# Performance work log

Measured on AMD Instinct MI355X. Metric: run time of the kernel, lower is better.

## Reference

```python
import jax, jax.numpy as jnp
import numpy as np

D_STATE = 64
D_CONV = 4
DT_RANK = 16  # ceil(256/16)
LN_EPS = 1e-5


def _mamba_layer(x, ln_g, ln_b, in_w, conv_w, conv_b, xp_w, dt_w, dt_b, A_log, Dp, out_w):
    B, L, d_model = x.shape
    # LayerNorm (pre-norm)
    mu = x.mean(-1, keepdims=True)
    var = ((x - mu) ** 2).mean(-1, keepdims=True)
    xn = (x - mu) * jax.lax.rsqrt(var + LN_EPS) * ln_g + ln_b
    # in_proj -> split into x-branch and gate z
    xz = xn @ in_w.T                    # [B,L,2*d_inner]
    xm, z = jnp.split(xz, 2, axis=-1)   # each [B,L,d_inner]
    d_inner = xm.shape[-1]
    # causal depthwise conv1d (kernel D_CONV), then SiLU
    xp = jnp.pad(xm, ((0, 0), (D_CONV - 1, 0), (0, 0)))
    xc = conv_b + sum(xp[:, k:k + L, :] * conv_w[:, k] for k in range(D_CONV))
    xc = jax.nn.silu(xc)
    # input-dependent SSM params
    dbl = xc @ xp_w.T                   # [B,L,dt_rank+2*N]
    dt, Bm, Cm = jnp.split(dbl, [DT_RANK, DT_RANK + D_STATE], axis=-1)
    dt = jax.nn.softplus(dt @ dt_w.T + dt_b)   # [B,L,d_inner]
    A = -jnp.exp(A_log)                 # [d_inner, N]

    def step(h, inp):
        dt_t, B_t, C_t, u_t = inp       # [B,Di],[B,N],[B,N],[B,Di]
        dA = jnp.exp(dt_t[:, :, None] * A)                 # [B,Di,N]
        dBu = (dt_t * u_t)[:, :, None] * B_t[:, None, :]   # [B,Di,N]
        h = dA * h + dBu
        y = jnp.einsum('bdn,bn->bd', h, C_t)
        return h, y

    h0 = jnp.zeros((B, d_inner, D_STATE), x.dtype)
    _, ys = jax.lax.scan(
        step, h0,
        (dt.transpose(1, 0, 2), Bm.transpose(1, 0, 2), Cm.transpose(1, 0, 2), xc.transpose(1, 0, 2)))
    y = ys.transpose(1, 0, 2) + xc * Dp  # skip term D*u
    y = y * jax.nn.silu(z)               # gating
    out = y @ out_w.T                    # out_proj
    return out + x                       # residual


def reference(x, ln_g, ln_b, in_w, conv_w, conv_b, xp_w, dt_w, dt_b, A_log, Dp, out_w):
    depth = ln_g.shape[0]
    for i in range(depth):
        x = _mamba_layer(x, ln_g[i], ln_b[i], in_w[i], conv_w[i], conv_b[i],
                         xp_w[i], dt_w[i], dt_b[i], A_log[i], Dp[i], out_w[i])
    return x


def setup_inputs() -> dict:
    key = jax.random.key(0)
    ks = jax.random.split(key, 8)
    B, L, d_model, depth = 4, 1024, 256, 2
    d_inner = 2 * d_model
    x = jax.random.normal(ks[0], (B, L, d_model), jnp.float32)
    s = 0.02
    in_w = jax.random.normal(ks[1], (depth, 2 * d_inner, d_model), jnp.float32) * s
    conv_w = jax.random.normal(ks[2], (depth, d_inner, D_CONV), jnp.float32) * 0.3
    conv_b = jnp.zeros((depth, d_inner), jnp.float32)
    xp_w = jax.random.normal(ks[3], (depth, DT_RANK + 2 * D_STATE, d_inner), jnp.float32) * s
    dt_w = jax.random.normal(ks[4], (depth, d_inner, DT_RANK), jnp.float32) * 0.1
    # inverse-softplus of ~0.01 so dt starts small (mamba-style init)
    dt_b = jnp.full((depth, d_inner), float(np.log(np.expm1(0.01))), jnp.float32)
    # A = diag(1..N) per channel -> A_log = log(arange)
    A_log = jnp.broadcast_to(jnp.log(jnp.arange(1, D_STATE + 1, dtype=jnp.float32)),
                             (depth, d_inner, D_STATE))
    Dp = jnp.ones((depth, d_inner), jnp.float32)
    out_w = jax.random.normal(ks[5], (depth, d_model, d_inner), jnp.float32) * s
    ln_g = jnp.ones((depth, d_model), jnp.float32)
    ln_b = jnp.zeros((depth, d_model), jnp.float32)
    return {"x": x, "ln_g": ln_g, "ln_b": ln_b, "in_w": in_w, "conv_w": conv_w,
            "conv_b": conv_b, "xp_w": xp_w, "dt_w": dt_w, "dt_b": dt_b,
            "A_log": A_log, "Dp": Dp, "out_w": out_w}
```

## Files before the change

### kernel.cpp

```cpp
#include <hip/hip_runtime.h>
#include <math.h>

#define DI 512
#define DM 256
#define LSEQ 1024
#define BB 4
#define NST 64
#define ROWS (BB*LSEQ)
#define NC 16
#define CL 64

typedef __bf16 bf16x8 __attribute__((ext_vector_type(8)));
typedef __bf16 bf16x4 __attribute__((ext_vector_type(4)));
typedef float f32x4 __attribute__((ext_vector_type(4)));
typedef unsigned short u16;
typedef u16 u16x8 __attribute__((ext_vector_type(8)));
typedef int i32x2 __attribute__((ext_vector_type(2)));

__device__ __forceinline__ float siluf(float x) { return x / (1.f + __expf(-x)); }
__device__ __forceinline__ float softplusf(float x) { return (x > 20.f) ? x : log1pf(__expf(x)); }
__device__ __forceinline__ float rlane(float v, int l) {
    return __int_as_float(__builtin_amdgcn_readlane(__float_as_int(v), l));
}
__device__ __forceinline__ float fexp2(float x) {
#if __has_builtin(__builtin_amdgcn_exp2f)
    return __builtin_amdgcn_exp2f(x);
#else
    return __expf(x * 0.69314718056f);
#endif
}
template<int PAT>
__device__ __forceinline__ float fswz(float v) {
    return __int_as_float(__builtin_amdgcn_ds_swizzle(__float_as_int(v), PAT));
}

__device__ __forceinline__ float tree8(const float (&s)[8], int lane) {
    const bool b4 = (lane & 16) != 0;
    const bool b3 = (lane & 8) != 0;
    float r[4];
#if __has_builtin(__builtin_amdgcn_permlane32_swap)
    #pragma unroll
    for (int i = 0; i < 4; ++i) {
        i32x2 pr = __builtin_amdgcn_permlane32_swap(
            __float_as_int(s[i]), __float_as_int(s[i+4]), false, false);
        r[i] = __int_as_float(pr[0]) + __int_as_float(pr[1]);
    }
#else
    const bool b5 = (lane & 32) != 0;
    #pragma unroll
    for (int i = 0; i < 4; ++i) {
        float u = b5 ? s[i+4] : s[i];
        float w = b5 ? s[i]   : s[i+4];
        r[i] = u + __shfl_xor(w, 32, 64);
    }
#endif
    float q[2];
    #pragma unroll
    for (int i = 0; i < 2; ++i) {
        float u = b4 ? r[i+2] : r[i];
        float w = b4 ? r[i]   : r[i+2];
        q[i] = u + fswz<0x401F>(w);
    }
    float u = b3 ? q[1] : q[0];
    float w = b3 ? q[0] : q[1];
    float p = u + fswz<0x201F>(w);
    p += fswz<0x101F>(p);
    p += fswz<0x081F>(p);
    p += fswz<0x041F>(p);
    return p;
}

__global__ __launch_bounds__(256) void f2bf(
    const float* __restrict__ in, __bf16* __restrict__ out, int n)
{
    int i = (blockIdx.x * 256 + threadIdx.x) * 4;
    if (i >= n) return;
    float4 v = *(const float4*)(in + i);
    bf16x4 o;
    o[0] = (__bf16)v.x; o[1] = (__bf16)v.y; o[2] = (__bf16)v.z; o[3] = (__bf16)v.w;
    *(bf16x4*)(out + i) = o;
}

__global__ __launch_bounds__(256) void ln_kernel(
    const float* __restrict__ x, const float* __restrict__ g,
    const float* __restrict__ b, __bf16* __restrict__ xn)
{
    int lane = threadIdx.x & 63;
    int row = blockIdx.x * 4 + (threadIdx.x >> 6);
    const float4* xr = (const float4*)(x + (size_t)row * DM);
    float4 v = xr[lane];
    float s = v.x + v.y + v.z + v.w;
    #pragma unroll
    for (int o = 32; o; o >>= 1) s += __shfl_xor(s, o, 64);
    float mu = s * (1.f / DM);
    float dx = v.x - mu, dy = v.y - mu, dz = v.z - mu, dw = v.w - mu;
    float q = dx*dx + dy*dy + dz*dz + dw*dw;
    #pragma unroll
    for (int o = 32; o; o >>= 1) q += __shfl_xor(q, o, 64);
    float inv = rsqrtf(q * (1.f / DM) + 1e-5f);
    float4 gv = ((const float4*)g)[lane];
    float4 bv = ((const float4*)b)[lane];
    bf16x4 o4;
    o4[0] = (__bf16)(dx * inv * gv.x + bv.x);
    o4[1] = (__bf16)(dy * inv * gv.y + bv.y);
    o4[2] = (__bf16)(dz * inv * gv.z + bv.z);
    o4[3] = (__bf16)(dw * inv * gv.w + bv.w);
    *(bf16x4*)(xn + (size_t)row * DM + lane * 4) = o4;
}

template<int KK>
__global__ __launch_bounds__(256) void gemm_mfma(
    const __bf16* __restrict__ A, const __bf16* __restrict__ W,
    float* __restrict__ C, __bf16* __restrict__ C2b,
    const float* __restrict__ res, int N, int mode)
{
    int wid = threadIdx.x >> 6, lane = threadIdx.x & 63;
    int wr = wid >> 1, wc = wid & 1;
    int bm = blockIdx.y * 64, bn = blockIdx.x * 64;
    int l15 = lane & 15, lk = (lane >> 4) * 8;
    const __bf16* Ap = A + (size_t)(bm + wr*32 + l15) * KK + lk;
    int wrow0 = bn + wc*32 + l15;
    int wrow1 = wrow0 + 16;
    if (wrow0 > N-1) wrow0 = N-1;
    if (wrow1 > N-1) wrow1 = N-1;
    const __bf16* Wp0 = W + (size_t)wrow0 * KK + lk;
    const __bf16* Wp1 = W + (size_t)wrow1 * KK + lk;
    f32x4 acc[2][2] = {};
    #pragma unroll 4
    for (int k0 = 0; k0 < KK; k0 += 32) {
        bf16x8 b0 = *(const bf16x8*)(Wp0 + k0);
        bf16x8 b1 = *(const bf16x8*)(Wp1 + k0);
        #pragma unroll
        for (int m = 0; m < 2; ++m) {
            bf16x8 a = *(const bf16x8*)(Ap + (size_t)m*16*KK + k0);
            acc[m][0] = __builtin_amdgcn_mfma_f32_16x16x32_bf16(a, b0, acc[m][0], 0, 0, 0);
            acc[m][1] = __builtin_amdgcn_mfma_f32_16x16x32_bf16(a, b1, acc[m][1], 0, 0, 0);
        }
    }
    int r4 = (lane >> 4) * 4;
    #pragma unroll
    for (int m = 0; m < 2; ++m) {
        int row = bm + wr*32 + m*16 + r4;
        #pragma unroll
        for (int n = 0; n < 2; ++n) {
            int col = bn + wc*32 + n*16 + l15;
            #pragma unroll
            for (int r = 0; r < 4; ++r) {
                float v = acc[m][n][r];
                int rr = row + r;
                if (mode == 0) {
                    if (col < N) C[(size_t)rr * N + col] = v;
                } else if (mode == 1) {
                    if (col < 512) C[(size_t)rr * 512 + col] = v;
                    else           C2b[(size_t)rr * 512 + col - 512] = (__bf16)v;
                } else {
                    C[(size_t)rr * N + col] = v + res[(size_t)rr * N + col];
                }
            }
        }
    }
}

__global__ __launch_bounds__(256) void gemm_dt(
    const float* __restrict__ A, int lda,
    const float* __restrict__ W,
    float* __restrict__ CT, const float* __restrict__ aux)
{
    __shared__ float As[16][68];
    __shared__ float Ws[16][68];
    const int bm = blockIdx.y * 64;
    const int bn = blockIdx.x * 64;
    const int tid = threadIdx.x;
    const int tx = tid & 15;
    const int ty = tid >> 4;
    const int lr = tid >> 2;
    const int lc = (tid & 3) << 2;
    float acc[4][4] = {};
    {
        float4 av = *(const float4*)(A + (size_t)(bm + lr) * lda + lc);
        float4 wv = *(const float4*)(W + (size_t)(bn + lr) * 16 + lc);
        As[lc+0][lr] = av.x; As[lc+1][lr] = av.y; As[lc+2][lr] = av.z; As[lc+3][lr] = av.w;
        Ws[lc+0][lr] = wv.x; Ws[lc+1][lr] = wv.y; Ws[lc+2][lr] = wv.z; Ws[lc+3][lr] = wv.w;
        __syncthreads();
        #pragma unroll
        for (int k = 0; k < 16; ++k) {
            float a[4], w[4];
            #pragma unroll
            for (int i = 0; i < 4; ++i) a[i] = As[k][ty*4 + i];
            #pragma unroll
            for (int j = 0; j < 4; ++j) w[j] = Ws[k][tx*4 + j];
            #pragma unroll
            for (int i = 0; i < 4; ++i)
                #pragma unroll
                for (int j = 0; j < 4; ++j)
                    acc[i][j] = fmaf(a[i], w[j], acc[i][j]);
        }
    }
    #pragma unroll
    for (int j = 0; j < 4; ++j) {
        int n = bn + tx*4 + j;
        float bia = aux[n];
        float4 v;
        v.x = softplusf(acc[0][j] + bia);
        v.y = softplusf(acc[1][j] + bia);
        v.z = softplusf(acc[2][j] + bia);
        v.w = softplusf(acc[3][j] + bia);
        *(float4*)(CT + (size_t)n * ROWS + bm + ty*4) = v;
    }
}

__global__ __launch_bounds__(256) void conv_tr_kernel(
    const float* __restrict__ xm, const float* __restrict__ cw,
    const float* __restrict__ cb, const u16* __restrict__ zin,
    __bf16* __restrict__ xcb, u16* __restrict__ xcT, u16* __restrict__ zT)
{
    __shared__ float xs[67][66];
    __shared__ u16 Tc[64][72];
    __shared__ u16 Tz[64][72];
    const int tid = threadIdx.x;
    const int row0 = blockIdx.y * 64;
    const int d0 = blockIdx.x * 64;
    #pragma unroll
    for (int it = 0; it < 5; ++it) {
        int f4 = it * 256 + tid;
        if (f4 < 67 * 16) {
            int rr = f4 >> 4;
            int cc = (f4 & 15) * 4;
            int g = row0 - 3 + rr;
            float4 v = make_float4(0.f, 0.f, 0.f, 0.f);
            if (g >= 0 && (g >> 10) == (row0 >> 10))
                v = *(const float4*)(xm + (size_t)g * DI + d0 + cc);
            *(float4*)&xs[rr][cc] = v;
        }
    }
    const int r = tid >> 2;
    const int c0 = (tid & 3) * 16;
    {
        const u16* zp = zin + (size_t)(row0 + r) * DI + d0 + c0;
        *(u16x8*)&Tz[r][c0]     = *(const u16x8*)(zp);
        *(u16x8*)&Tz[r][c0 + 8] = *(const u16x8*)(zp + 8);
    }
    __syncthreads();
    {
        bf16x8 v0, v1;
        #pragma unroll
        for (int j = 0; j < 16; ++j) {
            int d = d0 + c0 + j;
            float acc = cb[d]
                + xs[r+0][c0+j] * cw[d*4+0]
                + xs[r+1][c0+j] * cw[d*4+1]
                + xs[r+2][c0+j] * cw[d*4+2]
                + xs[r+3][c0+j] * cw[d*4+3];
            __bf16 o = (__bf16)siluf(acc);
            if (j < 8) v0[j] = o; else v1[j-8] = o;
            Tc[r][c0+j] = *(const u16*)&o;
        }
        __bf16* op = xcb + (size_t)(row0 + r) * DI + d0 + c0;
        *(bf16x8*)(op)     = v0;
        *(bf16x8*)(op + 8) = v1;
    }
    __syncthreads();
    {
        u16x8 a0, a1, b0, b1;
        #pragma unroll
        for (int i = 0; i < 8; ++i) {
            a0[i] = Tc[c0+i][r];   a1[i] = Tc[c0+8+i][r];
            b0[i] = Tz[c0+i][r];   b1[i] = Tz[c0+8+i][r];
        }
        u16* oc = xcT + (size_t)(d0 + r) * ROWS + row0 + c0;
        u16* oz = zT  + (size_t)(d0 + r) * ROWS + row0 + c0;
        *(u16x8*)(oc)     = a0;
        *(u16x8*)(oc + 8) = a1;
        *(u16x8*)(oz)     = b0;
        *(u16x8*)(oz + 8) = b1;
    }
}

__global__ __launch_bounds__(256) void transpose_bf(
    const u16* __restrict__ in, u16* __restrict__ out, int ldi, int ldo)
{
    __shared__ u16 tile[64][72];
    int r = threadIdx.x >> 2;
    int c0 = (threadIdx.x & 3) * 16;
    const u16* ip = in + (size_t)(blockIdx.y*64 + r) * ldi + blockIdx.x*64 + c0;
    *(u16x8*)&tile[r][c0]     = *(const u16x8*)(ip);
    *(u16x8*)&tile[r][c0 + 8] = *(const u16x8*)(ip + 8);
    __syncthreads();
    u16* op = out + (size_t)(blockIdx.x*64 + r) * ldo + blockIdx.y*64 + c0;
    u16x8 v0, v1;
    #pragma unroll
    for (int i = 0; i < 8; ++i) { v0[i] = tile[c0+i][r]; v1[i] = tile[c0+8+i][r]; }
    *(u16x8*)(op)     = v0;
    *(u16x8*)(op + 8) = v1;
}

__global__ __launch_bounds__(256) void scan_p1T(
    const float* __restrict__ dtT, const __bf16* __restrict__ xcT,
    const float* __restrict__ dbl, const float* __restrict__ A_log,
    float* __restrict__ Pe, float* __restrict__ He)
{
    int wid = (blockIdx.x * 256 + threadIdx.x) >> 6;
    int lane = threadIdx.x & 63;
    int c = wid & (NC - 1);
    int d = (wid >> 4) & (DI - 1);
    int b = wid >> 13;
    float An2 = -__expf(A_log[d * NST + lane]) * 1.44269504f;
    size_t row0 = (size_t)b * LSEQ + (size_t)c * CL;
    size_t tix = (size_t)d * ROWS + row0;
    float dtv = dtT[tix + lane];
    float uvf = (float)xcT[tix + lane];
    float duv = dtv * uvf;
    float Sdt = dtv;
    #pragma unroll
    for (int o = 32; o; o >>= 1) Sdt += __shfl_xor(Sdt, o, 64);
    const float* bp = dbl + row0 * 144 + 16 + lane;
    float H = 0.f;
    #pragma unroll
    for (int j = 0; j < 8; ++j) {
        #pragma unroll
        for (int q = 0; q < 8; ++q) {
            const int t = 8*j + q;
            float dA = fexp2(rlane(dtv, t) * An2);
            H = fmaf(dA, H, rlane(duv, t) * bp[q * 144]);
        }
        bp += 8 * 144;
    }
    size_t o = (size_t)wid * 64 + lane;
    Pe[o] = fexp2(An2 * Sdt);
    He[o] = H;
}

__global__ __launch_bounds__(256) void scan_p2T(
    const float* __restrict__ dtT, const __bf16* __restrict__ xcT,
    const __bf16* __restrict__ zT, const float* __restrict__ dbl,
    const float* __restrict__ A_log, const float* __restrict__ Dp,
    const float* __restrict__ Pe, const float* __restrict__ He,
    __bf16* __restrict__ yT)
{
    __shared__ float Ys[4][64];
    int wid = (blockIdx.x * 256 + threadIdx.x) >> 6;
    int w = threadIdx.x >> 6;
    int lane = threadIdx.x & 63;
    int c = wid & (NC - 1);
    int d = (wid >> 4) & (DI - 1);
    int b = wid >> 13;
    float An2 = -__expf(A_log[d * NST + lane]) * 1.44269504f;
    size_t row0 = (size_t)b * LSEQ + (size_t)c * CL;
    size_t tix = (size_t)d * ROWS + row0;
    float dtv = dtT[tix + lane];
    float uvf = (float)xcT[tix + lane];
    float zvf = (float)zT[tix + lane];
    float duv = dtv * uvf;
    float gD  = uvf * Dp[d];
    float wz  = siluf(zvf);
    float h = 0.f;
    {
        int cbase = wid - c;
        for (int j = 0; j < c; ++j) {
            size_t o = (size_t)(cbase + j) * 64 + lane;
            h = fmaf(Pe[o], h, He[o]);
        }
    }
    const float* bp = dbl + row0 * 144 + 16 + lane;
    const float* cp = dbl + row0 * 144 + 80 + lane;
    float yred[8];
    #pragma unroll
    for (int j = 0; j < 8; ++j) {
        float s[8];
        #pragma unroll
        for (int q = 0; q < 8; ++q) {
            const int t = 8*j + q;
            float dA = fexp2(rlane(dtv, t) * An2);
            h = fmaf(dA, h, rlane(duv, t) * bp[q * 144]);
            s[q] = h * cp[q * 144];
        }
        yred[j] = tree8(s, lane);
        bp += 8 * 144;
        cp += 8 * 144;
    }
    if ((lane & 7) == 0) {
        #pragma unroll
        for (int j = 0; j < 8; ++j) Ys[w][8*j + (lane >> 3)] = yred[j];
    }
    float y = (Ys[w][lane] + gD) * wz;
    yT[tix + lane] = (__bf16)y;
}

extern "C" void kernel_launch(void* const* d_in, const int* in_sizes, int n_in,
                              void* d_out, int out_size, void* d_ws, size_t ws_size,
                              hipStream_t stream)
{
    const float* x      = (const float*)d_in[0];
    const float* ln_g   = (const float*)d_in[1];
    const float* ln_b   = (const float*)d_in[2];
    const float* in_w   = (const float*)d_in[3];
    const float* conv_w = (const float*)d_in[4];
    const float* conv_b = (const float*)d_in[5];
    const float* xp_w   = (const float*)d_in[6];
    const float* dt_w   = (const float*)d_in[7];
    const float* dt_b   = (const float*)d_in[8];
    const float* A_log  = (const float*)d_in[9];
    const float* Dp     = (const float*)d_in[10];
    const float* out_w  = (const float*)d_in[11];
    float* out = (float*)d_out;

    char* ws = (char*)d_ws;
    const size_t MB = 1u << 20;
    float*  xm   = (float*)(ws + 0*MB);
    float*  Pe   = (float*)(ws + 0*MB);
    float*  dtT  = (float*)(ws + 8*MB);
    __bf16* xcbf = (__bf16*)(ws + 16*MB);
    __bf16* yTb  = (__bf16*)(ws + 16*MB);
    __bf16* xcT  = (__bf16*)(ws + 20*MB);
    __bf16* zbf  = (__bf16*)(ws + 24*MB);
    __bf16* ybf  = (__bf16*)(ws + 24*MB);
    __bf16* zT   = (__bf16*)(ws + 28*MB);
    float*  He   = (float*)(ws + 32*MB);
    float*  dblb = (float*)(ws + 40*MB);
    __bf16* xnb  = (__bf16*)(ws + 43*MB);
    __bf16* w_in  = (__bf16*)(ws + 45*MB);
    __bf16* w_xp  = (__bf16*)(ws + 46*MB);
    __bf16* w_out = (__bf16*)(ws + 46*MB + 512*1024);

    f2bf<<<512, 256, 0, stream>>>(in_w,  w_in,  2*1024*DM);
    f2bf<<<144, 256, 0, stream>>>(xp_w,  w_xp,  2*144*DI);
    f2bf<<<256, 256, 0, stream>>>(out_w, w_out, 2*DM*DI);

    for (int l = 0; l < 2; ++l) {
        const float* xin = (l == 0) ? x : out;
        ln_kernel<<<ROWS/4, 256, 0, stream>>>(xin, ln_g + l*DM, ln_b + l*DM, xnb);
        gemm_mfma<DM><<<dim3(1024/64, ROWS/64), 256, 0, stream>>>(
            xnb, w_in + (size_t)l*1024*DM, xm, zbf, nullptr, 1024, 1);
        conv_tr_kernel<<<dim3(DI/64, ROWS/64), 256, 0, stream>>>(
            xm, conv_w + (size_t)l*DI*4, conv_b + (size_t)l*DI,
            (const u16*)zbf, xcbf, (u16*)xcT, (u16*)zT);
        gemm_mfma<DI><<<dim3(3, ROWS/64), 256, 0, stream>>>(
            xcbf, w_xp + (size_t)l*144*DI, dblb, nullptr, nullptr, 144, 0);
        gemm_dt<<<dim3(DI/64, ROWS/64), 256, 0, stream>>>(
            dblb, 144, dt_w + (size_t)l*DI*16, dtT, dt_b + (size_t)l*DI);
        scan_p1T<<<(BB*DI*NC)/4, 256, 0, stream>>>(
            dtT, xcT, dblb, A_log + (size_t)l*DI*NST, Pe, He);
        scan_p2T<<<(BB*DI*NC)/4, 256, 0, stream>>>(
            dtT, xcT, zT, dblb, A_log + (size_t)l*DI*NST, Dp + (size_t)l*DI,
            Pe, He, yTb);
        transpose_bf<<<dim3(ROWS/64, DI/64), 256, 0, stream>>>(
            (const u16*)yTb, (u16*)ybf, ROWS, DI);
        gemm_mfma<DI><<<dim3(DM/64, ROWS/64), 256, 0, stream>>>(
            ybf, w_out + (size_t)l*DM*DI, out, nullptr, xin, DM, 2);
    }
}
```

Before: 314.6 us.

## Fuse two-pass chunked scan into one block-per-channel kernel, merge weight casts

The two chunked-scan kernels become one kernel where each block owns one (batch, channel) pair. Its four waves compute chunk summaries for the first 12 chunks into shared memory, then each wave combines the prefix and runs the output pass over its 4 chunks. This drops the global Pe/He round trip and one launch. In exchange the work per block is serialised, since each wave processes 3 plus 4 chunks in sequence and the grid is much smaller, so there is less parallelism to hide latency. The three weight-cast launches are also merged into a single launch.

```diff
diff --git a/kernel.cpp b/kernel.cpp
--- a/kernel.cpp
+++ b/kernel.cpp
@@ -70,15 +70,27 @@
     return p;
 }
 
-__global__ __launch_bounds__(256) void f2bf(
-    const float* __restrict__ in, __bf16* __restrict__ out, int n)
+__global__ __launch_bounds__(256) void f2bf3(
+    const float* __restrict__ a, __bf16* __restrict__ da, int na,
+    const float* __restrict__ b, __bf16* __restrict__ db, int nb,
+    const float* __restrict__ c, __bf16* __restrict__ dc, int nc)
 {
     int i = (blockIdx.x * 256 + threadIdx.x) * 4;
-    if (i >= n) return;
-    float4 v = *(const float4*)(in + i);
+    const float* src; __bf16* dst;
+    if (i < na) { src = a + i; dst = da + i; }
+    else {
+        i -= na;
+        if (i < nb) { src = b + i; dst = db + i; }
+        else {
+            i -= nb;
+            if (i >= nc) return;
+            src = c + i; dst = dc + i;
+        }
+    }
+    float4 v = *(const float4*)src;
     bf16x4 o;
     o[0] = (__bf16)v.x; o[1] = (__bf16)v.y; o[2] = (__bf16)v.z; o[3] = (__bf16)v.w;
-    *(bf16x4*)(out + i) = o;
+    *(bf16x4*)dst = o;
 }
 
 __global__ __launch_bounds__(256) void ln_kernel(
@@ -294,96 +306,90 @@
     *(u16x8*)(op + 8) = v1;
 }
 
-__global__ __launch_bounds__(256) void scan_p1T(
-    const float* __restrict__ dtT, const __bf16* __restrict__ xcT,
-    const float* __restrict__ dbl, const float* __restrict__ A_log,
-    float* __restrict__ Pe, float* __restrict__ He)
-{
-    int wid = (blockIdx.x * 256 + threadIdx.x) >> 6;
-    int lane = threadIdx.x & 63;
-    int c = wid & (NC - 1);
-    int d = (wid >> 4) & (DI - 1);
-    int b = wid >> 13;
-    float An2 = -__expf(A_log[d * NST + lane]) * 1.44269504f;
-    size_t row0 = (size_t)b * LSEQ + (size_t)c * CL;
-    size_t tix = (size_t)d * ROWS + row0;
-    float dtv = dtT[tix + lane];
-    float uvf = (float)xcT[tix + lane];
-    float duv = dtv * uvf;
-    float Sdt = dtv;
-    #pragma unroll
-    for (int o = 32; o; o >>= 1) Sdt += __shfl_xor(Sdt, o, 64);
-    const float* bp = dbl + row0 * 144 + 16 + lane;
-    float H = 0.f;
-    #pragma unroll
-    for (int j = 0; j < 8; ++j) {
-        #pragma unroll
-        for (int q = 0; q < 8; ++q) {
-            const int t = 8*j + q;
-            float dA = fexp2(rlane(dtv, t) * An2);
-            H = fmaf(dA, H, rlane(duv, t) * bp[q * 144]);
-        }
-        bp += 8 * 144;
-    }
-    size_t o = (size_t)wid * 64 + lane;
-    Pe[o] = fexp2(An2 * Sdt);
-    He[o] = H;
-}
-
-__global__ __launch_bounds__(256) void scan_p2T(
+__global__ __launch_bounds__(256) void scan_fused2(
     const float* __restrict__ dtT, const __bf16* __restrict__ xcT,
     const __bf16* __restrict__ zT, const float* __restrict__ dbl,
     const float* __restrict__ A_log, const float* __restrict__ Dp,
-    const float* __restrict__ Pe, const float* __restrict__ He,
     __bf16* __restrict__ yT)
 {
+    __shared__ float Pa[12][NST];
+    __shared__ float Ha[12][NST];
     __shared__ float Ys[4][64];
-    int wid = (blockIdx.x * 256 + threadIdx.x) >> 6;
-    int w = threadIdx.x >> 6;
-    int lane = threadIdx.x & 63;
-    int c = wid & (NC - 1);
-    int d = (wid >> 4) & (DI - 1);
-    int b = wid >> 13;
-    float An2 = -__expf(A_log[d * NST + lane]) * 1.44269504f;
-    size_t row0 = (size_t)b * LSEQ + (size_t)c * CL;
-    size_t tix = (size_t)d * ROWS + row0;
-    float dtv = dtT[tix + lane];
-    float uvf = (float)xcT[tix + lane];
-    float zvf = (float)zT[tix + lane];
-    float duv = dtv * uvf;
-    float gD  = uvf * Dp[d];
-    float wz  = siluf(zvf);
+    const int w = threadIdx.x >> 6;
+    const int lane = threadIdx.x & 63;
+    const int d = blockIdx.x & (DI - 1);
+    const int b = blockIdx.x >> 9;
+    const float An2 = -__expf(A_log[d * NST + lane]) * 1.44269504f;
+    const float dpd = Dp[d];
+    const size_t rowb = (size_t)b * LSEQ;
+    const size_t tixb = (size_t)d * ROWS + rowb;
+
+    #pragma unroll 1
+    for (int cc = 0; cc < 3; ++cc) {
+        const int c = w * 3 + cc;
+        const size_t tix = tixb + (size_t)c * CL;
+        float dtv = dtT[tix + lane];
+        float uvf = (float)xcT[tix + lane];
+        float duv = dtv * uvf;
+        float Sdt = dtv;
+        #pragma unroll
+        for (int o = 32; o; o >>= 1) Sdt += __shfl_xor(Sdt, o, 64);
+        const float* bp = dbl + (rowb + (size_t)c * CL) * 144 + 16 + lane;
+        float H = 0.f;
+        #pragma unroll
+        for (int j = 0; j < 8; ++j) {
+            #pragma unroll
+            for (int q = 0; q < 8; ++q) {
+                const int t = 8*j + q;
+                float dA = fexp2(rlane(dtv, t) * An2);
+                H = fmaf(dA, H, rlane(duv, t) * bp[q * 144]);
+            }
+            bp += 8 * 144;
+        }
+        Pa[c][lane] = fexp2(An2 * Sdt);
+        Ha[c][lane] = H;
+    }
+    __syncthreads();
+
     float h = 0.f;
-    {
-        int cbase = wid - c;
-        for (int j = 0; j < c; ++j) {
-            size_t o = (size_t)(cbase + j) * 64 + lane;
-            h = fmaf(Pe[o], h, He[o]);
-        }
-    }
-    const float* bp = dbl + row0 * 144 + 16 + lane;
-    const float* cp = dbl + row0 * 144 + 80 + lane;
-    float yred[8];
-    #pragma unroll
-    for (int j = 0; j < 8; ++j) {
-        float s[8];
-        #pragma unroll
-        for (int q = 0; q < 8; ++q) {
-            const int t = 8*j + q;
-            float dA = fexp2(rlane(dtv, t) * An2);
-            h = fmaf(dA, h, rlane(duv, t) * bp[q * 144]);
-            s[q] = h * cp[q * 144];
-        }
-        yred[j] = tree8(s, lane);
-        bp += 8 * 144;
-        cp += 8 * 144;
-    }
-    if ((lane & 7) == 0) {
-        #pragma unroll
-        for (int j = 0; j < 8; ++j) Ys[w][8*j + (lane >> 3)] = yred[j];
-    }
-    float y = (Ys[w][lane] + gD) * wz;
-    yT[tix + lane] = (__bf16)y;
+    #pragma unroll 1
+    for (int j = 0; j < w * 4; ++j)
+        h = fmaf(Pa[j][lane], h, Ha[j][lane]);
+
+    #pragma unroll 1
+    for (int cc = 0; cc < 4; ++cc) {
+        const int c = w * 4 + cc;
+        const size_t tix = tixb + (size_t)c * CL;
+        float dtv = dtT[tix + lane];
+        float uvf = (float)xcT[tix + lane];
+        float zvf = (float)zT[tix + lane];
+        float duv = dtv * uvf;
+        float gD  = uvf * dpd;
+        float wz  = siluf(zvf);
+        const float* bp = dbl + (rowb + (size_t)c * CL) * 144 + 16 + lane;
+        const float* cp = bp + 64;
+        float yred[8];
+        #pragma unroll
+        for (int j = 0; j < 8; ++j) {
+            float s[8];
+            #pragma unroll
+            for (int q = 0; q < 8; ++q) {
+                const int t = 8*j + q;
+                float dA = fexp2(rlane(dtv, t) * An2);
+                h = fmaf(dA, h, rlane(duv, t) * bp[q * 144]);
+                s[q] = h * cp[q * 144];
+            }
+            yred[j] = tree8(s, lane);
+            bp += 8 * 144;
+            cp += 8 * 144;
+        }
+        if ((lane & 7) == 0) {
+            #pragma unroll
+            for (int j = 0; j < 8; ++j) Ys[w][8*j + (lane >> 3)] = yred[j];
+        }
+        float y = (Ys[w][lane] + gD) * wz;
+        yT[tix + lane] = (__bf16)y;
+    }
 }
 
 extern "C" void kernel_launch(void* const* d_in, const int* in_sizes, int n_in,
@@ -407,7 +413,6 @@
     char* ws = (char*)d_ws;
     const size_t MB = 1u << 20;
     float*  xm   = (float*)(ws + 0*MB);
-    float*  Pe   = (float*)(ws + 0*MB);
     float*  dtT  = (float*)(ws + 8*MB);
     __bf16* xcbf = (__bf16*)(ws + 16*MB);
     __bf16* yTb  = (__bf16*)(ws + 16*MB);
@@ -415,16 +420,15 @@
     __bf16* zbf  = (__bf16*)(ws + 24*MB);
     __bf16* ybf  = (__bf16*)(ws + 24*MB);
     __bf16* zT   = (__bf16*)(ws + 28*MB);
-    float*  He   = (float*)(ws + 32*MB);
     float*  dblb = (float*)(ws + 40*MB);
     __bf16* xnb  = (__bf16*)(ws + 43*MB);
     __bf16* w_in  = (__bf16*)(ws + 45*MB);
     __bf16* w_xp  = (__bf16*)(ws + 46*MB);
     __bf16* w_out = (__bf16*)(ws + 46*MB + 512*1024);
 
-    f2bf<<<512, 256, 0, stream>>>(in_w,  w_in,  2*1024*DM);
-    f2bf<<<144, 256, 0, stream>>>(xp_w,  w_xp,  2*144*DI);
-    f2bf<<<256, 256, 0, stream>>>(out_w, w_out, 2*DM*DI);
+    const int na = 2*1024*DM, nb = 2*144*DI, nc = 2*DM*DI;
+    f2bf3<<<(na+nb+nc)/1024, 256, 0, stream>>>(
+        in_w, w_in, na, xp_w, w_xp, nb, out_w, w_out, nc);
 
     for (int l = 0; l < 2; ++l) {
         const float* xin = (l == 0) ? x : out;
@@ -438,11 +442,8 @@
             xcbf, w_xp + (size_t)l*144*DI, dblb, nullptr, nullptr, 144, 0);
         gemm_dt<<<dim3(DI/64, ROWS/64), 256, 0, stream>>>(
             dblb, 144, dt_w + (size_t)l*DI*16, dtT, dt_b + (size_t)l*DI);
-        scan_p1T<<<(BB*DI*NC)/4, 256, 0, stream>>>(
-            dtT, xcT, dblb, A_log + (size_t)l*DI*NST, Pe, He);
-        scan_p2T<<<(BB*DI*NC)/4, 256, 0, stream>>>(
-            dtT, xcT, zT, dblb, A_log + (size_t)l*DI*NST, Dp + (size_t)l*DI,
-            Pe, He, yTb);
+        scan_fused2<<<BB*DI, 256, 0, stream>>>(
+            dtT, xcT, zT, dblb, A_log + (size_t)l*DI*NST, Dp + (size_t)l*DI, yTb);
         transpose_bf<<<dim3(ROWS/64, DI/64), 256, 0, stream>>>(
             (const u16*)yTb, (u16*)ybf, ROWS, DI);
         gemm_mfma<DI><<<dim3(DM/64, ROWS/64), 256, 0, stream>>>(
```

Result: faster. 288.0 us (-8.5%).
